# Kernel tuning notes

Hardware: AMD Instinct MI355X
Metric: run time of the kernel (lower is better)

## Reference

```python
import jax, jax.numpy as jnp
import numpy as np

HID = 256  # hidden_dim


def setup_inputs() -> dict:
    key = jax.random.key(0)
    ks = jax.random.split(key, 8)
    B, C, H, W = 256, 1, 1024, 64
    D = W  # input_dim
    scale = 0.05
    return {
        "x": jax.random.normal(ks[0], (B, C, H, W), jnp.float32),
        "h0": jax.random.normal(ks[1], (B, HID), jnp.float32),
        "c0": jax.random.normal(ks[2], (B, HID), jnp.float32),
        "Wi": jax.random.normal(ks[3], (4 * HID, D), jnp.float32) * scale,
        "bi": jnp.zeros((4 * HID,), jnp.float32),
        "Wh": jax.random.normal(ks[4], (4 * HID, HID), jnp.float32) * scale,
        "bh": jnp.zeros((4 * HID,), jnp.float32),
        "Wcls": jax.random.normal(ks[5], (10, HID), jnp.float32) * scale,
        "bcls": jnp.zeros((10,), jnp.float32),
    }


def reference(x, h0, c0, Wi, bi, Wh, bh, Wcls, bcls):
    B, C, H, W = x.shape
    S = C * H  # seq_length
    seq = x.reshape(B, S, W)
    # precompute input-to-gate projections for all timesteps: [B,S,4H]
    xg = jnp.einsum("bsd,gd->bsg", seq, Wi) + bi

    def step(carry, xg_t):
        h, c = carry
        g = xg_t + h @ Wh.T + bh  # [B,4H], gate order: f,i,g,o
        f = jax.nn.sigmoid(g[:, 0 * HID:1 * HID])
        i = jax.nn.sigmoid(g[:, 1 * HID:2 * HID])
        gg = jnp.tanh(g[:, 2 * HID:3 * HID])
        o = jax.nn.sigmoid(g[:, 3 * HID:4 * HID])
        c_new = c * f + i * gg
        h_new = jnp.tanh(c_new) * o
        return (h_new, c_new), None

    (h_last, _), _ = jax.lax.scan(step, (h0, c0), jnp.swapaxes(xg, 0, 1))
    # classifier on last hidden state
    return h_last @ Wcls.T + bcls
```

## Files before the change

### kernel.cpp

```cpp
#include <hip/hip_runtime.h>

#define SEQ   1024
#define DIN   64
#define NHID  256
#define NBLK  64
#define NTHR  512

typedef _Float16 f16x8 __attribute__((ext_vector_type(8)));
typedef float    f32x4 __attribute__((ext_vector_type(4)));
typedef unsigned long long u64;

#define MFMA16(a,b,c) __builtin_amdgcn_mfma_f32_16x16x32_f16((a),(b),(c),0,0,0)
#define ALOAD(p)    __hip_atomic_load((p), __ATOMIC_RELAXED, __HIP_MEMORY_SCOPE_AGENT)
#define ASTORE(p,v) __hip_atomic_store((p),(v), __ATOMIC_RELAXED, __HIP_MEMORY_SCOPE_AGENT)

__device__ __forceinline__ float sigm(float v){
  return __builtin_amdgcn_rcpf(1.f + __expf(-v));
}
__device__ __forceinline__ float tanh_f(float v){
  return 1.f - 2.f*__builtin_amdgcn_rcpf(__expf(2.f*v)+1.f);
}

__device__ __forceinline__ f16x8 cvt8(f32x4 a, f32x4 b){
  f16x8 r;
  r[0]=(_Float16)a[0]; r[1]=(_Float16)a[1]; r[2]=(_Float16)a[2]; r[3]=(_Float16)a[3];
  r[4]=(_Float16)b[0]; r[5]=(_Float16)b[1]; r[6]=(_Float16)b[2]; r[7]=(_Float16)b[3];
  return r;
}

union U32H2 { unsigned int u; _Float16 h[2]; unsigned short us[2]; };

__global__ void __launch_bounds__(NTHR, 2)
lstm_seq(const float* __restrict__ x, const float* __restrict__ h0,
         const float* __restrict__ c0, const float* __restrict__ Wi,
         const float* __restrict__ bi, const float* __restrict__ Wh,
         const float* __restrict__ bh, const float* __restrict__ Wcls,
         const float* __restrict__ bcls,
         u64* __restrict__ slices, float* __restrict__ out)
{
  __shared__ __align__(16) unsigned int hbuf[2][16*128];

  const int bid = blockIdx.x;
  const int grp = bid & 15;
  const int q   = bid >> 4;
  const int tid = threadIdx.x;
  const int w   = tid >> 6;
  const int l   = tid & 63;
  const int l15 = l & 15;
  const int lhi = l >> 4;

  f16x8 wa[2][8], xa[2][2];
#pragma unroll
  for (int t=0;t<2;t++){
    const int mt  = w*2 + t;
    const int mr  = l15;
    const int jl  = (mt>>1)*8 + ((mr>>2)<<1) + (mt&1);
    const int row = (mr&3)*NHID + q*64 + jl;
#pragma unroll
    for (int kt=0;kt<8;kt++){
      const float* p = Wh + row*NHID + kt*32 + lhi*8;
      wa[t][kt] = cvt8(*(const f32x4*)p, *(const f32x4*)(p+4));
    }
#pragma unroll
    for (int kt=0;kt<2;kt++){
      const float* p = Wi + row*DIN + kt*32 + lhi*8;
      xa[t][kt] = cvt8(*(const f32x4*)p, *(const f32x4*)(p+4));
    }
  }

  f32x4 binit0, binit1; float c[2];
#pragma unroll
  for (int t=0;t<2;t++){
    const int jl = w*8 + lhi*2 + t;
    f32x4 bv;
#pragma unroll
    for (int g=0; g<4; g++)
      bv[g] = bi[g*NHID + q*64 + jl] + bh[g*NHID + q*64 + jl];
    if (t==0) binit0 = bv; else binit1 = bv;
    c[t] = c0[(size_t)(grp*16+l15)*NHID + q*64 + jl];
  }

  for (int i=tid; i<16*128; i+=NTHR){
    const int b = i>>7, cp = i&127;
    U32H2 pk;
    pk.h[0] = (_Float16)h0[(size_t)(grp*16+b)*NHID + cp*2];
    pk.h[1] = (_Float16)h0[(size_t)(grp*16+b)*NHID + cp*2 + 1];
    hbuf[0][i ^ ((b&7)<<2)] = pk.u;
  }
  __syncthreads();

  const float* xrow = x + (size_t)(grp*16 + l15) * (SEQ*DIN);
  f32x4 xp0,xp1,xp2,xp3;
  {
    const float* p = xrow + lhi*8;
    xp0 = *(const f32x4*)p;      xp1 = *(const f32x4*)(p+4);
    xp2 = *(const f32x4*)(p+32); xp3 = *(const f32x4*)(p+36);
  }
  f32x4 acc0, acc1;
  {
    f16x8 xb0 = cvt8(xp0, xp1), xb1 = cvt8(xp2, xp3);
    acc0 = MFMA16(xa[0][0], xb0, binit0);
    acc0 = MFMA16(xa[0][1], xb1, acc0);
    acc1 = MFMA16(xa[1][0], xb0, binit1);
    acc1 = MFMA16(xa[1][1], xb1, acc1);
  }
  {
    const float* p = xrow + DIN + lhi*8;
    xp0 = *(const f32x4*)p;      xp1 = *(const f32x4*)(p+4);
    xp2 = *(const f32x4*)(p+32); xp3 = *(const f32x4*)(p+36);
  }

  for (int s=0; s<SEQ; s++){
    const unsigned int* hr = hbuf[s&1];
    unsigned int*       hw_= hbuf[(s+1)&1];
    u64* base = slices + (size_t)((s&1)*NBLK + grp*4)*512;
    const unsigned tag = (unsigned)(s+1);

    f16x8 hb[8];
#pragma unroll
    for (int kt=0;kt<8;kt++){
      const int word = (l15*128 + kt*16 + lhi*4) ^ ((l15&7)<<2);
      hb[kt] = *(const f16x8*)(hr + word);
    }
    f32x4 a0 = acc0, a1 = acc1;
    f32x4 b0 = {0.f,0.f,0.f,0.f}, b1 = {0.f,0.f,0.f,0.f};
#pragma unroll
    for (int kt=0;kt<4;kt++){
      a0 = MFMA16(wa[0][kt],   hb[kt],   a0);
      a1 = MFMA16(wa[1][kt],   hb[kt],   a1);
      b0 = MFMA16(wa[0][kt+4], hb[kt+4], b0);
      b1 = MFMA16(wa[1][kt+4], hb[kt+4], b1);
    }
    const f32x4 g0 = a0 + b0, g1 = a1 + b1;

    U32H2 pk;
    {
      const float f0 = sigm (g0[0]);
      const float i0 = sigm (g0[1]);
      const float gg0= tanh_f(g0[2]);
      const float o0 = sigm (g0[3]);
      c[0] = c[0]*f0 + i0*gg0;
      pk.h[0] = (_Float16)(tanh_f(c[0])*o0);
      const float f1 = sigm (g1[0]);
      const float i1 = sigm (g1[1]);
      const float gg1= tanh_f(g1[2]);
      const float o1 = sigm (g1[3]);
      c[1] = c[1]*f1 + i1*gg1;
      pk.h[1] = (_Float16)(tanh_f(c[1])*o1);
    }

    const int wo = w*64 + l;
    const int qA=(q+1)&3, qB=(q+2)&3, qC=(q+3)&3;
    const u64* pA = base + qA*512 + wo;
    const u64* pB = base + qB*512 + wo;
    const u64* pC = base + qC*512 + wo;
    ASTORE(base + q*512 + wo, ((u64)tag << 32) | (u64)pk.u);
    u64 vA = ALOAD(pA);
    u64 vB = ALOAD(pB);
    u64 vC = ALOAD(pC);
    __builtin_amdgcn_sched_barrier(0);

    {
      const int jp = w*4 + lhi;
      hw_[(l15*128 + q*32 + jp) ^ ((l15&7)<<2)] = pk.u;
    }
    {
      f16x8 xb0 = cvt8(xp0, xp1), xb1 = cvt8(xp2, xp3);
      acc0 = MFMA16(xa[0][0], xb0, binit0);
      acc0 = MFMA16(xa[0][1], xb1, acc0);
      acc1 = MFMA16(xa[1][0], xb0, binit1);
      acc1 = MFMA16(xa[1][1], xb1, acc1);
    }
    {
      const int sn = (s < SEQ-2) ? s+2 : SEQ-1;
      const float* p = xrow + sn*DIN + lhi*8;
      xp0 = *(const f32x4*)p;      xp1 = *(const f32x4*)(p+4);
      xp2 = *(const f32x4*)(p+32); xp3 = *(const f32x4*)(p+36);
    }

    bool dA = ((unsigned)(vA>>32) == tag);
    bool dB = ((unsigned)(vB>>32) == tag);
    bool dC = ((unsigned)(vC>>32) == tag);
    while (!(dA && dB && dC)){
      u64 nA, nB, nC;
      if (!dA) nA = ALOAD(pA);
      if (!dB) nB = ALOAD(pB);
      if (!dC) nC = ALOAD(pC);
      if (!dA && (unsigned)(nA>>32) == tag){ vA = nA; dA = true; }
      if (!dB && (unsigned)(nB>>32) == tag){ vB = nB; dB = true; }
      if (!dC && (unsigned)(nC>>32) == tag){ vC = nC; dC = true; }
    }
    {
      const int jp = w*4 + lhi;
      hw_[(l15*128 + qA*32 + jp) ^ ((l15&7)<<2)] = (unsigned)vA;
      hw_[(l15*128 + qB*32 + jp) ^ ((l15&7)<<2)] = (unsigned)vB;
      hw_[(l15*128 + qC*32 + jp) ^ ((l15&7)<<2)] = (unsigned)vC;
    }
    __syncthreads();
  }

  if (q == 0 && tid < 160){
    const int b = tid/10, j = tid - b*10;
    const unsigned int* hf = hbuf[SEQ&1];
    float sum = bcls[j];
    for (int cp=0; cp<128; cp++){
      U32H2 v; v.u = hf[(b*128 + cp) ^ ((b&7)<<2)];
      sum += Wcls[j*NHID + cp*2]     * (float)v.h[0]
           + Wcls[j*NHID + cp*2 + 1] * (float)v.h[1];
    }
    out[(grp*16+b)*10 + j] = sum;
  }
}

extern "C" void kernel_launch(void* const* d_in, const int* in_sizes, int n_in,
                              void* d_out, int out_size, void* d_ws, size_t ws_size,
                              hipStream_t stream){
  const float* x    = (const float*)d_in[0];
  const float* h0   = (const float*)d_in[1];
  const float* c0   = (const float*)d_in[2];
  const float* Wi   = (const float*)d_in[3];
  const float* bi   = (const float*)d_in[4];
  const float* Wh   = (const float*)d_in[5];
  const float* bh   = (const float*)d_in[6];
  const float* Wcls = (const float*)d_in[7];
  const float* bcls = (const float*)d_in[8];

  u64* slices = (u64*)d_ws;

  hipMemsetAsync(slices, 0, 2*NBLK*512*sizeof(u64), stream);
  hipLaunchKernelGGL(lstm_seq, dim3(NBLK), dim3(NTHR), 0, stream,
                     x, h0, c0, Wi, bi, Wh, bh, Wcls, bcls,
                     slices, (float*)d_out);
}
```

Measured before the change: 2.346 ms.

## Interleave per-block h slices so one vector load polls all four peers

Result: faster. 2.141 ms (-8.7%).

```diff
diff --git a/kernel.cpp b/kernel.cpp
--- a/kernel.cpp
+++ b/kernel.cpp
@@ -8,11 +8,18 @@
 
 typedef _Float16 f16x8 __attribute__((ext_vector_type(8)));
 typedef float    f32x4 __attribute__((ext_vector_type(4)));
+typedef unsigned int u32;
+typedef u32      u32x4 __attribute__((ext_vector_type(4)));
 typedef unsigned long long u64;
 
 #define MFMA16(a,b,c) __builtin_amdgcn_mfma_f32_16x16x32_f16((a),(b),(c),0,0,0)
-#define ALOAD(p)    __hip_atomic_load((p), __ATOMIC_RELAXED, __HIP_MEMORY_SCOPE_AGENT)
 #define ASTORE(p,v) __hip_atomic_store((p),(v), __ATOMIC_RELAXED, __HIP_MEMORY_SCOPE_AGENT)
+#define PLOAD(d, b, O) \
+  asm volatile("global_load_dwordx4 %0, %1, off offset:" #O " sc0 sc1" \
+               : "=v"(d) : "v"(b) : "memory")
+#define WAITBIND2(a,b) do{ \
+  asm volatile("s_waitcnt vmcnt(0)" : "+v"(a), "+v"(b) :: "memory"); \
+  __builtin_amdgcn_sched_barrier(0); }while(0)
 
 __device__ __forceinline__ float sigm(float v){
   return __builtin_amdgcn_rcpf(1.f + __expf(-v));
@@ -28,7 +35,7 @@
   return r;
 }
 
-union U32H2 { unsigned int u; _Float16 h[2]; unsigned short us[2]; };
+union U32H2 { u32 u; _Float16 h[2]; unsigned short us[2]; };
 
 __global__ void __launch_bounds__(NTHR, 2)
 lstm_seq(const float* __restrict__ x, const float* __restrict__ h0,
@@ -38,7 +45,7 @@
          const float* __restrict__ bcls,
          u64* __restrict__ slices, float* __restrict__ out)
 {
-  __shared__ __align__(16) unsigned int hbuf[2][16*128];
+  __shared__ __align__(16) u32 hbuf[2][16*128];
 
   const int bid = blockIdx.x;
   const int grp = bid & 15;
@@ -110,10 +117,12 @@
     xp2 = *(const f32x4*)(p+32); xp3 = *(const f32x4*)(p+36);
   }
 
+  const int pos = w*64 + l;
+
   for (int s=0; s<SEQ; s++){
-    const unsigned int* hr = hbuf[s&1];
-    unsigned int*       hw_= hbuf[(s+1)&1];
-    u64* base = slices + (size_t)((s&1)*NBLK + grp*4)*512;
+    const u32* hr = hbuf[s&1];
+    u32*       hw_= hbuf[(s+1)&1];
+    u64* base = slices + (size_t)((s&1)*16 + grp)*2048;
     const unsigned tag = (unsigned)(s+1);
 
     f16x8 hb[8];
@@ -149,21 +158,9 @@
       pk.h[1] = (_Float16)(tanh_f(c[1])*o1);
     }
 
-    const int wo = w*64 + l;
-    const int qA=(q+1)&3, qB=(q+2)&3, qC=(q+3)&3;
-    const u64* pA = base + qA*512 + wo;
-    const u64* pB = base + qB*512 + wo;
-    const u64* pC = base + qC*512 + wo;
-    ASTORE(base + q*512 + wo, ((u64)tag << 32) | (u64)pk.u);
-    u64 vA = ALOAD(pA);
-    u64 vB = ALOAD(pB);
-    u64 vC = ALOAD(pC);
+    ASTORE(base + pos*4 + q, ((u64)tag << 32) | (u64)pk.u);
     __builtin_amdgcn_sched_barrier(0);
 
-    {
-      const int jp = w*4 + lhi;
-      hw_[(l15*128 + q*32 + jp) ^ ((l15&7)<<2)] = pk.u;
-    }
     {
       f16x8 xb0 = cvt8(xp0, xp1), xb1 = cvt8(xp2, xp3);
       acc0 = MFMA16(xa[0][0], xb0, binit0);
@@ -178,30 +175,27 @@
       xp2 = *(const f32x4*)(p+32); xp3 = *(const f32x4*)(p+36);
     }
 
-    bool dA = ((unsigned)(vA>>32) == tag);
-    bool dB = ((unsigned)(vB>>32) == tag);
-    bool dC = ((unsigned)(vC>>32) == tag);
-    while (!(dA && dB && dC)){
-      u64 nA, nB, nC;
-      if (!dA) nA = ALOAD(pA);
-      if (!dB) nB = ALOAD(pB);
-      if (!dC) nC = ALOAD(pC);
-      if (!dA && (unsigned)(nA>>32) == tag){ vA = nA; dA = true; }
-      if (!dB && (unsigned)(nB>>32) == tag){ vB = nB; dB = true; }
-      if (!dC && (unsigned)(nC>>32) == tag){ vC = nC; dC = true; }
+    const u64* pp = base + pos*4;
+    u32x4 lo, hi;
+    PLOAD(lo, pp, 0); PLOAD(hi, pp, 16);
+    WAITBIND2(lo, hi);
+    while (lo[1]!=tag || lo[3]!=tag || hi[1]!=tag || hi[3]!=tag){
+      PLOAD(lo, pp, 0); PLOAD(hi, pp, 16);
+      WAITBIND2(lo, hi);
     }
     {
       const int jp = w*4 + lhi;
-      hw_[(l15*128 + qA*32 + jp) ^ ((l15&7)<<2)] = (unsigned)vA;
-      hw_[(l15*128 + qB*32 + jp) ^ ((l15&7)<<2)] = (unsigned)vB;
-      hw_[(l15*128 + qC*32 + jp) ^ ((l15&7)<<2)] = (unsigned)vC;
+      hw_[(l15*128 +       jp) ^ ((l15&7)<<2)] = lo[0];
+      hw_[(l15*128 +  32 + jp) ^ ((l15&7)<<2)] = lo[2];
+      hw_[(l15*128 +  64 + jp) ^ ((l15&7)<<2)] = hi[0];
+      hw_[(l15*128 +  96 + jp) ^ ((l15&7)<<2)] = hi[2];
     }
     __syncthreads();
   }
 
   if (q == 0 && tid < 160){
     const int b = tid/10, j = tid - b*10;
-    const unsigned int* hf = hbuf[SEQ&1];
+    const u32* hf = hbuf[SEQ&1];
     float sum = bcls[j];
     for (int cp=0; cp<128; cp++){
       U32H2 v; v.u = hf[(b*128 + cp) ^ ((b&7)<<2)];
@@ -227,7 +221,7 @@
 
   u64* slices = (u64*)d_ws;
 
-  hipMemsetAsync(slices, 0, 2*NBLK*512*sizeof(u64), stream);
+  hipMemsetAsync(slices, 0, (size_t)2*16*512*4*sizeof(u64), stream);
   hipLaunchKernelGGL(lstm_seq, dim3(NBLK), dim3(NTHR), 0, stream,
                      x, h0, c0, Wi, bi, Wh, bh, Wcls, bcls,
                      slices, (float*)d_out);
```
